# Performance work log

Hardware: AMD Instinct MI355X
Metric: run time of the kernel (lower is better)

Reference implementation:

```python
import jax, jax.numpy as jnp
import numpy as np

B, T, D, H = 2, 2048, 2048, 32
HD = D // H
# quantization scales (constructor-time attributes in the original repo)
A_PROJ = 3e-4   # q/k/v proj alpha (W8A8B8O8Linear)
A_QK = 2e-5     # qk_bmm alpha (BMM_S8T_S8N_F32T)
A_PV = 1e-2     # pv_bmm alpha (BMM_S8T_S8N_S8T)
A_OUT = 1e-4    # out_proj alpha (W8A8BFP32OFP32Linear)


def _i8(key, shape):
    return jax.random.randint(key, shape, -128, 128, dtype=jnp.int32).astype(jnp.int8)


def setup_inputs() -> dict:
    key = jax.random.key(0)
    ks = jax.random.split(key, 10)
    hidden_states = _i8(ks[0], (B, T, D))
    # causal mask, 0 on/below diagonal, large negative above
    causal = jnp.triu(jnp.full((T, T), -1e9, dtype=jnp.float32), k=1)
    attention_mask = jnp.broadcast_to(causal, (B, 1, T, T))
    return {
        "hidden_states": hidden_states,
        "attention_mask": attention_mask,
        "Wq": _i8(ks[1], (D, D)), "bq": _i8(ks[2], (D,)),
        "Wk": _i8(ks[3], (D, D)), "bk": _i8(ks[4], (D,)),
        "Wv": _i8(ks[5], (D, D)), "bv": _i8(ks[6], (D,)),
        "Wo": _i8(ks[7], (D, D)),
        "bo": jax.random.normal(ks[8], (D,), dtype=jnp.float32),
    }


def _w8a8b8o8(x_i8, W_i8, b_i8, alpha):
    # int8 GEMM -> int32 accum; epilogue: alpha*acc + bias, saturate to int8
    acc = jnp.einsum('btk,nk->btn', x_i8.astype(jnp.int32), W_i8.astype(jnp.int32))
    y = alpha * acc.astype(jnp.float32) + b_i8.astype(jnp.float32)
    return jnp.clip(jnp.round(y), -128, 127).astype(jnp.int8)


def reference(hidden_states, attention_mask, Wq, bq, Wk, bk, Wv, bv, Wo, bo):
    # q/k/v projections: int8 in, int8 out
    q = _w8a8b8o8(hidden_states, Wq, bq, A_PROJ)
    k = _w8a8b8o8(hidden_states, Wk, bk, A_PROJ)
    v = _w8a8b8o8(hidden_states, Wv, bv, A_PROJ)

    def shape(x):  # [B,T,D] -> [B,H,T,HD]
        return x.reshape(B, T, H, HD).transpose(0, 2, 1, 3)

    qh, kh, vh = shape(q), shape(k), shape(v)

    # qk_bmm (BMM_S8T_S8N_F32T): fp32 = alpha * int8 q @ k^T
    attn = A_QK * jnp.einsum('bhtd,bhsd->bhts',
                             qh.astype(jnp.int32), kh.astype(jnp.int32)).astype(jnp.float32)
    attn = attn + attention_mask  # [B,1,T,T] broadcasts over heads
    attn = jnp.maximum(attn, jnp.finfo(jnp.float32).min)
    probs = jax.nn.softmax(attn, axis=-1)

    # quantize probs: p.mul_(127).round_() -> int8
    p_i8 = jnp.clip(jnp.round(probs * 127.0), -128, 127).astype(jnp.int8)

    # pv_bmm (BMM_S8T_S8N_S8T): int8 out = sat(round(alpha * p @ v))
    pv = jnp.einsum('bhts,bhsd->bhtd', p_i8.astype(jnp.int32), vh.astype(jnp.int32))
    attn_out_i8 = jnp.clip(jnp.round(A_PV * pv.astype(jnp.float32)), -128, 127).astype(jnp.int8)

    # [B,H,T,HD] -> [B,T,D]
    attn_out = attn_out_i8.transpose(0, 2, 1, 3).reshape(B, T, D)

    # out_proj (W8A8BFP32OFP32Linear): fp32 = alpha*(x@W^T) + fp32 bias
    acc = jnp.einsum('btk,nk->btn', attn_out.astype(jnp.int32), Wo.astype(jnp.int32))
    out = A_OUT * acc.astype(jnp.float32) + bo
    return out
```

## Files before the change

kernel.cpp:

```cpp
#include <hip/hip_runtime.h>
#include <cstdint>

#define A_PROJ 3e-4f
#define A_QK   2e-5f
#define A_PV   1e-2f
#define A_OUT  1e-4f

#define NB 2
#define NT 2048
#define ND 2048
#define NH 32
#define NHD 64
#define NM (NB*NT)

typedef int v4i __attribute__((ext_vector_type(4)));

__device__ __forceinline__ int8_t sat8(float y) {
  float r = rintf(y);
  r = fminf(fmaxf(r, -128.f), 127.f);
  return (int8_t)(int)r;
}

__device__ __forceinline__ float exp2_fast(float x) {
  return __builtin_amdgcn_exp2f(x);
}

__device__ __forceinline__ void gl2lds16(const int8_t* g, int8_t* l) {
  __builtin_amdgcn_global_load_lds(
      (const __attribute__((address_space(1))) void*)g,
      (__attribute__((address_space(3))) void*)l, 16, 0, 0);
}

__device__ __forceinline__ uint32_t pack_lo4(float f0, float f1, float f2, float f3) {
  uint32_t u0 = __float_as_uint(f0), u1 = __float_as_uint(f1);
  uint32_t u2 = __float_as_uint(f2), u3 = __float_as_uint(f3);
  uint32_t lo = __builtin_amdgcn_perm(u1, u0, 0x04000400u);
  uint32_t hi = __builtin_amdgcn_perm(u3, u2, 0x04000400u);
  return __builtin_amdgcn_perm(hi, lo, 0x05040100u);
}

__device__ __forceinline__ void xcd_map(int lid, int& bx, int& by) {
  int xcd = lid & 7, j = lid >> 3;
  bx = (xcd & 3) * 8 + (j & 7);
  by = (xcd >> 2) * 8 + (j >> 3);
}

#define NWW (ND*ND/4)
__global__ void pack_all(const int* __restrict__ X,
                         const int* __restrict__ W0, const int* __restrict__ W1,
                         const int* __restrict__ W2, const int* __restrict__ W3,
                         int8_t* __restrict__ dX, int8_t* __restrict__ dW0,
                         int8_t* __restrict__ dW1, int8_t* __restrict__ dW2,
                         int8_t* __restrict__ dW3) {
  int i = blockIdx.x * blockDim.x + threadIdx.x;
  const int nx = NM*ND/4;
  const int* src; int8_t* dst; int off;
  if (i < nx) { src = X; dst = dX; off = i; }
  else {
    int j = i - nx;
    int r = j >> 20;
    off = j & (NWW - 1);
    src = (r == 0) ? W0 : (r == 1) ? W1 : (r == 2) ? W2 : W3;
    dst = (r == 0) ? dW0 : (r == 1) ? dW1 : (r == 2) ? dW2 : dW3;
  }
  int4 v = ((const int4*)src)[off];
  uint32_t p = (uint32_t)(v.x & 255) | ((uint32_t)(v.y & 255) << 8) |
               ((uint32_t)(v.z & 255) << 16) | ((uint32_t)(v.w & 255) << 24);
  ((uint32_t*)dst)[off] = p;
}

__global__ __launch_bounds__(256, 2) void gemm_qkv(
    const int8_t* __restrict__ X,
    const int8_t* __restrict__ Wq, const int8_t* __restrict__ Wk, const int8_t* __restrict__ Wv,
    const int* __restrict__ bq, const int* __restrict__ bk, const int* __restrict__ bv,
    int8_t* __restrict__ Qh, int8_t* __restrict__ Kh, int8_t* __restrict__ Vt)
{
  __shared__ __align__(16) int8_t S[2][4][128][64];
  int bx, by;
  xcd_map(blockIdx.x + 32 * blockIdx.y, bx, by);
  const int m0 = bx * 128, n0 = by * 128;
  const int tid = threadIdx.x, lane = tid & 63, wave = tid >> 6;
  const int wm = wave >> 1, wn = wave & 1;
  const int l15 = lane & 15, quad = lane >> 4;

  const int srow = lane >> 2;
  const int scol = (((lane & 3) ^ ((lane >> 3) & 3)) * 16);
  const int rqcol = (quad ^ ((l15 >> 1) & 3)) * 16;

  const int8_t* srcp[8];
  int8_t* dstp[8];
  #pragma unroll
  for (int j = 0; j < 8; ++j) {
    int slot = j * 4 + wave;
    int rblk = slot & 7;
    int sel  = slot >> 3;
    int row  = rblk * 16 + srow;
    const int8_t* base = (sel == 0) ? &X[(size_t)(m0 + row) * ND]
                                    : (sel == 1) ? &Wq[(size_t)(n0 + row) * ND]
                                    : (sel == 2) ? &Wk[(size_t)(n0 + row) * ND]
                                                 : &Wv[(size_t)(n0 + row) * ND];
    srcp[j] = base + scol;
    dstp[j] = &S[0][sel][rblk * 16][0];
  }

  v4i acc[3][4][4];
  const v4i vzero = {0, 0, 0, 0};
  #pragma unroll
  for (int z = 0; z < 3; ++z)
    #pragma unroll
    for (int i = 0; i < 4; ++i)
      #pragma unroll
      for (int j = 0; j < 4; ++j) acc[z][i][j] = vzero;

  #pragma unroll
  for (int j = 0; j < 8; ++j) gl2lds16(srcp[j], dstp[j]);
  __syncthreads();

  int cur = 0;
  for (int k0 = 64; k0 <= ND; k0 += 64) {
    if (k0 < ND) {
      const int boff = (cur ^ 1) * 32768;
      #pragma unroll
      for (int j = 0; j < 8; ++j) gl2lds16(srcp[j] + k0, dstp[j] + boff);
    }
    v4i a[4];
    #pragma unroll
    for (int mt = 0; mt < 4; ++mt)
      a[mt] = *(const v4i*)&S[cur][0][wm*64 + mt*16 + l15][rqcol];
    #pragma unroll
    for (int z = 0; z < 3; ++z)
      #pragma unroll
      for (int nt = 0; nt < 4; ++nt) {
        v4i b = *(const v4i*)&S[cur][1 + z][wn*64 + nt*16 + l15][rqcol];
        #pragma unroll
        for (int mt = 0; mt < 4; ++mt)
          acc[z][mt][nt] = __builtin_amdgcn_mfma_i32_16x16x64_i8(a[mt], b, acc[z][mt][nt], 0, 0, 0);
      }
    __syncthreads();
    cur ^= 1;
  }

  #pragma unroll
  for (int z = 0; z < 3; ++z) {
    const int* bias = (z == 0) ? bq : (z == 1) ? bk : bv;
    float bf[4];
    #pragma unroll
    for (int nt = 0; nt < 4; ++nt) bf[nt] = (float)bias[n0 + wn*64 + nt*16 + l15];
    if (z == 2) {
      #pragma unroll
      for (int mt = 0; mt < 4; ++mt)
        #pragma unroll
        for (int nt = 0; nt < 4; ++nt) {
          int tbase = (m0 + wm*64 + mt*16 + quad*4) & (NT - 1);
          int bb = (m0 + wm*64) >> 11;
          int n = n0 + wn*64 + nt*16 + l15;
          int hh = n >> 6, hd = n & (NHD - 1);
          uint32_t pk = 0;
          #pragma unroll
          for (int r = 0; r < 4; ++r) {
            uint32_t q = (uint32_t)(uint8_t)sat8(A_PROJ * (float)acc[z][mt][nt][r] + bf[nt]);
            pk |= q << (8 * r);
          }
          size_t bh = (size_t)bb * NH + hh;
          *(uint32_t*)&Vt[(bh * NHD + hd) * NT + tbase] = pk;
        }
    } else {
      int8_t* O = (z == 0) ? Qh : Kh;
      #pragma unroll
      for (int mt = 0; mt < 4; ++mt)
        #pragma unroll
        for (int nt = 0; nt < 4; ++nt)
          #pragma unroll
          for (int r = 0; r < 4; ++r) {
            int m = m0 + wm*64 + mt*16 + quad*4 + r;
            int n = n0 + wn*64 + nt*16 + l15;
            int8_t q = sat8(A_PROJ * (float)acc[z][mt][nt][r] + bf[nt]);
            int bb = m >> 11, t = m & (NT - 1);
            int hh = n >> 6, hd = n & (NHD - 1);
            size_t bh = (size_t)bb * NH + hh;
            O[(bh * NT + t) * NHD + hd] = q;
          }
    }
  }
}

__global__ __launch_bounds__(512, 8) void attn_fused(
    const int8_t* __restrict__ Qh, const int8_t* __restrict__ Kh, const int8_t* __restrict__ Vt,
    int8_t* __restrict__ AO)
{
  __shared__ __align__(16) int8_t Ksd[2][64][64];
  __shared__ __align__(16) int8_t Vsd[2][64][64];
  __shared__ __align__(16) uint32_t Ps32[8][16][20];

  const int bx = blockIdx.x;
  const int bh = blockIdx.y;
  const int tid = threadIdx.x, lane = tid & 63, wave = tid >> 6;
  const int l15 = lane & 15, quad = lane >> 4;
  const v4i vzero = {0, 0, 0, 0};
  const float MAGIC = 12582912.0f;
  const float C2 = 2.8853900817779268e-05f;

  const int jg = bh >> 4;
  const int x = (jg == 0) ? bx : (jg == 1) ? (15 - bx)
              : (jg == 2) ? ((bx + 8) & 15) : ((7 - bx) & 15);

  const int8_t* Qp = Qh + (size_t)bh * NT * NHD;
  const int8_t* Kp = Kh + (size_t)bh * NT * NHD;
  const int8_t* Vp = Vt + (size_t)bh * NHD * NT;
  const int bb = bh >> 5, hhead = bh & (NH - 1);

  const int t0 = x * 128;
  const int nsteps = 2 * x + 2;
  const int tw = t0 + wave * 16;
  const int tme = tw + l15;

  const int strow = lane >> 2;
  const int stcol = (((lane & 3) ^ ((lane >> 3) & 3)) * 16);
  const int fcol  = (quad ^ ((l15 >> 1) & 3)) * 16;

  v4i qf = *(const v4i*)&Qp[(size_t)(tw + l15) * NHD + quad * 16];

  float ls0 = 0.f, ls1 = 0.f, ls2 = 0.f, ls3 = 0.f;
  if (wave < 4)
    gl2lds16(&Kp[(size_t)(0 + wave*16 + strow) * NHD + stcol], &Ksd[0][wave*16][0]);
  __syncthreads();
  int cur = 0;
  for (int st = 0; st < nsteps; ++st) {
    if (st + 1 < nsteps && wave < 4)
      gl2lds16(&Kp[(size_t)((st+1)*64 + wave*16 + strow) * NHD + stcol],
               &Ksd[cur ^ 1][wave*16][0]);
    const int s0 = st * 64;
    if (s0 <= tw + 15) {
      v4i kf[4];
      #pragma unroll
      for (int mt = 0; mt < 4; ++mt) kf[mt] = *(const v4i*)&Ksd[cur][mt*16 + l15][fcol];
      if (s0 + 63 <= tw) {
        #pragma unroll
        for (int mt = 0; mt < 4; ++mt) {
          v4i sa = __builtin_amdgcn_mfma_i32_16x16x64_i8(kf[mt], qf, vzero, 0, 0, 0);
          ls0 += exp2_fast(C2 * (float)sa[0]);
          ls1 += exp2_fast(C2 * (float)sa[1]);
          ls2 += exp2_fast(C2 * (float)sa[2]);
          ls3 += exp2_fast(C2 * (float)sa[3]);
        }
      } else {
        #pragma unroll
        for (int mt = 0; mt < 4; ++mt) {
          v4i sa = __builtin_amdgcn_mfma_i32_16x16x64_i8(kf[mt], qf, vzero, 0, 0, 0);
          const int sb = s0 + mt*16 + quad*4;
          ls0 += (sb + 0 <= tme) ? exp2_fast(C2 * (float)sa[0]) : 0.f;
          ls1 += (sb + 1 <= tme) ? exp2_fast(C2 * (float)sa[1]) : 0.f;
          ls2 += (sb + 2 <= tme) ? exp2_fast(C2 * (float)sa[2]) : 0.f;
          ls3 += (sb + 3 <= tme) ? exp2_fast(C2 * (float)sa[3]) : 0.f;
        }
      }
    }
    __syncthreads();
    cur ^= 1;
  }
  float lsum = (ls0 + ls1) + (ls2 + ls3);
  lsum += __shfl_xor(lsum, 16, 64);
  lsum += __shfl_xor(lsum, 32, 64);
  const float linv = 127.0f / lsum;

  v4i accv[4];
  #pragma unroll
  for (int jj = 0; jj < 4; ++jj) accv[jj] = vzero;

  if (wave < 4)
    gl2lds16(&Kp[(size_t)(0 + wave*16 + strow) * NHD + stcol], &Ksd[0][wave*16][0]);
  else
    gl2lds16(&Vp[(size_t)((wave-4)*16 + strow) * NT + 0 + stcol], &Vsd[0][(wave-4)*16][0]);
  __syncthreads();
  cur = 0;
  for (int st = 0; st < nsteps; ++st) {
    if (st + 1 < nsteps) {
      if (wave < 4)
        gl2lds16(&Kp[(size_t)((st+1)*64 + wave*16 + strow) * NHD + stcol],
                 &Ksd[cur ^ 1][wave*16][0]);
      else
        gl2lds16(&Vp[(size_t)((wave-4)*16 + strow) * NT + (st+1)*64 + stcol],
                 &Vsd[cur ^ 1][(wave-4)*16][0]);
    }
    const int s0 = st * 64;
    if (s0 <= tw + 15) {
      v4i kf[4];
      #pragma unroll
      for (int mt = 0; mt < 4; ++mt) kf[mt] = *(const v4i*)&Ksd[cur][mt*16 + l15][fcol];
      if (s0 + 63 <= tw) {
        #pragma unroll
        for (int mt = 0; mt < 4; ++mt) {
          v4i sa = __builtin_amdgcn_mfma_i32_16x16x64_i8(kf[mt], qf, vzero, 0, 0, 0);
          float f0 = fmaf(exp2_fast(C2 * (float)sa[0]), linv, MAGIC);
          float f1 = fmaf(exp2_fast(C2 * (float)sa[1]), linv, MAGIC);
          float f2 = fmaf(exp2_fast(C2 * (float)sa[2]), linv, MAGIC);
          float f3 = fmaf(exp2_fast(C2 * (float)sa[3]), linv, MAGIC);
          Ps32[wave][l15][mt*4 + quad] = pack_lo4(f0, f1, f2, f3);
        }
      } else {
        #pragma unroll
        for (int mt = 0; mt < 4; ++mt) {
          v4i sa = __builtin_amdgcn_mfma_i32_16x16x64_i8(kf[mt], qf, vzero, 0, 0, 0);
          const int sb = s0 + mt*16 + quad*4;
          float e0 = (sb + 0 <= tme) ? exp2_fast(C2 * (float)sa[0]) : 0.f;
          float e1 = (sb + 1 <= tme) ? exp2_fast(C2 * (float)sa[1]) : 0.f;
          float e2 = (sb + 2 <= tme) ? exp2_fast(C2 * (float)sa[2]) : 0.f;
          float e3 = (sb + 3 <= tme) ? exp2_fast(C2 * (float)sa[3]) : 0.f;
          Ps32[wave][l15][mt*4 + quad] =
              pack_lo4(fmaf(e0, linv, MAGIC), fmaf(e1, linv, MAGIC),
                       fmaf(e2, linv, MAGIC), fmaf(e3, linv, MAGIC));
        }
      }
      v4i ap = *(const v4i*)&Ps32[wave][l15][quad*4];
      #pragma unroll
      for (int nt2 = 0; nt2 < 4; ++nt2) {
        v4i bvv = *(const v4i*)&Vsd[cur][nt2*16 + l15][fcol];
        accv[nt2] = __builtin_amdgcn_mfma_i32_16x16x64_i8(ap, bvv, accv[nt2], 0, 0, 0);
      }
    }
    __syncthreads();
    cur ^= 1;
  }

  #pragma unroll
  for (int nt2 = 0; nt2 < 4; ++nt2)
    #pragma unroll
    for (int r = 0; r < 4; ++r) {
      int t = tw + quad*4 + r;
      int d = nt2*16 + l15;
      AO[((size_t)bb * NT + t) * ND + hhead * NHD + d] = sat8(A_PV * (float)accv[nt2][r]);
    }
}

__global__ __launch_bounds__(256) void gemm_out(
    const int8_t* __restrict__ X, const int8_t* __restrict__ W,
    const float* __restrict__ bo, float* __restrict__ out)
{
  __shared__ __align__(16) int8_t As[2][128][64];
  __shared__ __align__(16) int8_t Bs[2][128][64];
  int bx, by;
  xcd_map(blockIdx.x + 32 * blockIdx.y, bx, by);
  const int m0 = bx * 128, n0 = by * 128;
  const int tid = threadIdx.x, lane = tid & 63, wave = tid >> 6;
  const int wm = wave >> 1, wn = wave & 1;
  const int l15 = lane & 15, quad = lane >> 4;
  const int srow = lane >> 2;
  const int scol = (((lane & 3) ^ ((lane >> 3) & 3)) * 16);
  const int rqcol = (quad ^ ((l15 >> 1) & 3)) * 16;

  const int8_t* srcp[4];
  int8_t* dstp[4];
  #pragma unroll
  for (int j = 0; j < 4; ++j) {
    int slot = j * 4 + wave;
    int rblk = slot & 7;
    int row = rblk * 16 + srow;
    if (slot < 8) { srcp[j] = &X[(size_t)(m0 + row) * ND + scol]; dstp[j] = &As[0][rblk*16][0]; }
    else          { srcp[j] = &W[(size_t)(n0 + row) * ND + scol]; dstp[j] = &Bs[0][rblk*16][0]; }
  }

  v4i acc[4][4];
  const v4i vzero = {0, 0, 0, 0};
  #pragma unroll
  for (int i = 0; i < 4; ++i)
    #pragma unroll
    for (int j = 0; j < 4; ++j) acc[i][j] = vzero;

  #pragma unroll
  for (int j = 0; j < 4; ++j) gl2lds16(srcp[j], dstp[j]);
  __syncthreads();

  int cur = 0;
  for (int k0 = 64; k0 <= ND; k0 += 64) {
    if (k0 < ND) {
      const int boff = (cur ^ 1) * 8192;
      #pragma unroll
      for (int j = 0; j < 4; ++j) gl2lds16(srcp[j] + k0, dstp[j] + boff);
    }
    v4i a[4], b[4];
    #pragma unroll
    for (int mt = 0; mt < 4; ++mt) a[mt] = *(const v4i*)&As[cur][wm*64 + mt*16 + l15][rqcol];
    #pragma unroll
    for (int nt = 0; nt < 4; ++nt) b[nt] = *(const v4i*)&Bs[cur][wn*64 + nt*16 + l15][rqcol];
    #pragma unroll
    for (int mt = 0; mt < 4; ++mt)
      #pragma unroll
      for (int nt = 0; nt < 4; ++nt)
        acc[mt][nt] = __builtin_amdgcn_mfma_i32_16x16x64_i8(a[mt], b[nt], acc[mt][nt], 0, 0, 0);
    __syncthreads();
    cur ^= 1;
  }

  float bf[4];
  #pragma unroll
  for (int nt = 0; nt < 4; ++nt) bf[nt] = bo[n0 + wn*64 + nt*16 + l15];

  #pragma unroll
  for (int mt = 0; mt < 4; ++mt)
    #pragma unroll
    for (int nt = 0; nt < 4; ++nt)
      #pragma unroll
      for (int r = 0; r < 4; ++r) {
        int m = m0 + wm*64 + mt*16 + quad*4 + r;
        int n = n0 + wn*64 + nt*16 + l15;
        out[(size_t)m * ND + n] = A_OUT * (float)acc[mt][nt][r] + bf[nt];
      }
}

extern "C" void kernel_launch(void* const* d_in, const int* in_sizes, int n_in,
                              void* d_out, int out_size, void* d_ws, size_t ws_size,
                              hipStream_t stream)
{
  const int*   hs  = (const int*)d_in[0];
  const int*   Wq  = (const int*)d_in[2];
  const int*   bq  = (const int*)d_in[3];
  const int*   Wk  = (const int*)d_in[4];
  const int*   bkb = (const int*)d_in[5];
  const int*   Wv  = (const int*)d_in[6];
  const int*   bvb = (const int*)d_in[7];
  const int*   Wo  = (const int*)d_in[8];
  const float* bo  = (const float*)d_in[9];
  float* out = (float*)d_out;

  char* ws = (char*)d_ws;
  const size_t SZ_X = (size_t)NM * ND;
  const size_t SZ_W = (size_t)ND * ND;
  const size_t SZ_H = (size_t)NB * NH * NT * NHD;
  int8_t* Xp  = (int8_t*)ws;
  int8_t* Wqp = (int8_t*)(ws + SZ_X);
  int8_t* Wkp = Wqp + SZ_W;
  int8_t* Wvp = Wkp + SZ_W;
  int8_t* Wop = Wvp + SZ_W;
  int8_t* Qh  = Wop + SZ_W;
  int8_t* Kh  = Qh + SZ_H;
  int8_t* Vt  = Kh + SZ_H;
  int8_t* AO  = Xp;

  const int ntot = (int)(SZ_X/4 + 4 * (SZ_W/4));
  pack_all<<<(ntot + 255) / 256, 256, 0, stream>>>(hs, Wq, Wk, Wv, Wo,
                                                   Xp, Wqp, Wkp, Wvp, Wop);

  gemm_qkv<<<dim3(32, 16), 256, 0, stream>>>(Xp, Wqp, Wkp, Wvp, bq, bkb, bvb, Qh, Kh, Vt);
  attn_fused<<<dim3(16, NB*NH), 512, 0, stream>>>(Qh, Kh, Vt, AO);
  gemm_out<<<dim3(NM/128, ND/128), 256, 0, stream>>>(AO, Wop, bo, out);
}
```

Baseline: 304.4 us.

## Restructure attention blocks into paired 64-row query tiles for causal balance

Each attention block now has 256 threads (4 waves) and handles two 64-row query tiles, bx and 31-bx. Pairing them gives every block the same total causal work, replacing the previous per-head-group swizzle over 128-row tiles. All waves now load both K and V, and the per-wave skip check is no longer needed because tiles match the 64-wide key step. The trade-offs are a smaller block with fewer waves to hide latency and two serial passes per block.

Measured after the change: 308.8 us. Within noise of the previous version (+1.4%).

```diff
diff --git a/kernel.cpp b/kernel.cpp
--- a/kernel.cpp
+++ b/kernel.cpp
@@ -184,13 +184,13 @@
   }
 }
 
-__global__ __launch_bounds__(512, 8) void attn_fused(
+__global__ __launch_bounds__(256, 4) void attn_fused(
     const int8_t* __restrict__ Qh, const int8_t* __restrict__ Kh, const int8_t* __restrict__ Vt,
     int8_t* __restrict__ AO)
 {
   __shared__ __align__(16) int8_t Ksd[2][64][64];
   __shared__ __align__(16) int8_t Vsd[2][64][64];
-  __shared__ __align__(16) uint32_t Ps32[8][16][20];
+  __shared__ __align__(16) uint32_t Ps32[4][16][20];
 
   const int bx = blockIdx.x;
   const int bh = blockIdx.y;
@@ -200,50 +200,36 @@
   const float MAGIC = 12582912.0f;
   const float C2 = 2.8853900817779268e-05f;
 
-  const int jg = bh >> 4;
-  const int x = (jg == 0) ? bx : (jg == 1) ? (15 - bx)
-              : (jg == 2) ? ((bx + 8) & 15) : ((7 - bx) & 15);
-
   const int8_t* Qp = Qh + (size_t)bh * NT * NHD;
   const int8_t* Kp = Kh + (size_t)bh * NT * NHD;
   const int8_t* Vp = Vt + (size_t)bh * NHD * NT;
   const int bb = bh >> 5, hhead = bh & (NH - 1);
 
-  const int t0 = x * 128;
-  const int nsteps = 2 * x + 2;
-  const int tw = t0 + wave * 16;
-  const int tme = tw + l15;
-
   const int strow = lane >> 2;
   const int stcol = (((lane & 3) ^ ((lane >> 3) & 3)) * 16);
   const int fcol  = (quad ^ ((l15 >> 1) & 3)) * 16;
 
-  v4i qf = *(const v4i*)&Qp[(size_t)(tw + l15) * NHD + quad * 16];
-
-  float ls0 = 0.f, ls1 = 0.f, ls2 = 0.f, ls3 = 0.f;
-  if (wave < 4)
-    gl2lds16(&Kp[(size_t)(0 + wave*16 + strow) * NHD + stcol], &Ksd[0][wave*16][0]);
-  __syncthreads();
-  int cur = 0;
-  for (int st = 0; st < nsteps; ++st) {
-    if (st + 1 < nsteps && wave < 4)
-      gl2lds16(&Kp[(size_t)((st+1)*64 + wave*16 + strow) * NHD + stcol],
-               &Ksd[cur ^ 1][wave*16][0]);
-    const int s0 = st * 64;
-    if (s0 <= tw + 15) {
+  for (int half = 0; half < 2; ++half) {
+    const int x = half ? (31 - bx) : bx;
+    const int t0 = x * 64;
+    const int tw = t0 + wave * 16;
+    const int tme = tw + l15;
+
+    v4i qf = *(const v4i*)&Qp[(size_t)(tw + l15) * NHD + quad * 16];
+
+    float ls0 = 0.f, ls1 = 0.f, ls2 = 0.f, ls3 = 0.f;
+    gl2lds16(&Kp[(size_t)(wave*16 + strow) * NHD + stcol], &Ksd[0][wave*16][0]);
+    __syncthreads();
+    int cur = 0;
+    for (int st = 0; st <= x; ++st) {
+      if (st < x)
+        gl2lds16(&Kp[(size_t)((st+1)*64 + wave*16 + strow) * NHD + stcol],
+                 &Ksd[cur ^ 1][wave*16][0]);
+      const int s0 = st * 64;
       v4i kf[4];
       #pragma unroll
       for (int mt = 0; mt < 4; ++mt) kf[mt] = *(const v4i*)&Ksd[cur][mt*16 + l15][fcol];
-      if (s0 + 63 <= tw) {
-        #pragma unroll
-        for (int mt = 0; mt < 4; ++mt) {
-          v4i sa = __builtin_amdgcn_mfma_i32_16x16x64_i8(kf[mt], qf, vzero, 0, 0, 0);
-          ls0 += exp2_fast(C2 * (float)sa[0]);
-          ls1 += exp2_fast(C2 * (float)sa[1]);
-          ls2 += exp2_fast(C2 * (float)sa[2]);
-          ls3 += exp2_fast(C2 * (float)sa[3]);
-        }
-      } else {
+      if (st == x) {
         #pragma unroll
         for (int mt = 0; mt < 4; ++mt) {
           v4i sa = __builtin_amdgcn_mfma_i32_16x16x64_i8(kf[mt], qf, vzero, 0, 0, 0);
@@ -253,51 +239,44 @@
           ls2 += (sb + 2 <= tme) ? exp2_fast(C2 * (float)sa[2]) : 0.f;
           ls3 += (sb + 3 <= tme) ? exp2_fast(C2 * (float)sa[3]) : 0.f;
         }
-      }
+      } else {
+        #pragma unroll
+        for (int mt = 0; mt < 4; ++mt) {
+          v4i sa = __builtin_amdgcn_mfma_i32_16x16x64_i8(kf[mt], qf, vzero, 0, 0, 0);
+          ls0 += exp2_fast(C2 * (float)sa[0]);
+          ls1 += exp2_fast(C2 * (float)sa[1]);
+          ls2 += exp2_fast(C2 * (float)sa[2]);
+          ls3 += exp2_fast(C2 * (float)sa[3]);
+        }
+      }
+      __syncthreads();
+      cur ^= 1;
     }
+    float lsum = (ls0 + ls1) + (ls2 + ls3);
+    lsum += __shfl_xor(lsum, 16, 64);
+    lsum += __shfl_xor(lsum, 32, 64);
+    const float linv = 127.0f / lsum;
+
+    v4i accv[4];
+    #pragma unroll
+    for (int jj = 0; jj < 4; ++jj) accv[jj] = vzero;
+
+    gl2lds16(&Kp[(size_t)(wave*16 + strow) * NHD + stcol], &Ksd[0][wave*16][0]);
+    gl2lds16(&Vp[(size_t)(wave*16 + strow) * NT + stcol], &Vsd[0][wave*16][0]);
     __syncthreads();
-    cur ^= 1;
-  }
-  float lsum = (ls0 + ls1) + (ls2 + ls3);
-  lsum += __shfl_xor(lsum, 16, 64);
-  lsum += __shfl_xor(lsum, 32, 64);
-  const float linv = 127.0f / lsum;
-
-  v4i accv[4];
-  #pragma unroll
-  for (int jj = 0; jj < 4; ++jj) accv[jj] = vzero;
-
-  if (wave < 4)
-    gl2lds16(&Kp[(size_t)(0 + wave*16 + strow) * NHD + stcol], &Ksd[0][wave*16][0]);
-  else
-    gl2lds16(&Vp[(size_t)((wave-4)*16 + strow) * NT + 0 + stcol], &Vsd[0][(wave-4)*16][0]);
-  __syncthreads();
-  cur = 0;
-  for (int st = 0; st < nsteps; ++st) {
-    if (st + 1 < nsteps) {
-      if (wave < 4)
+    cur = 0;
+    for (int st = 0; st <= x; ++st) {
+      if (st < x) {
         gl2lds16(&Kp[(size_t)((st+1)*64 + wave*16 + strow) * NHD + stcol],
                  &Ksd[cur ^ 1][wave*16][0]);
-      else
-        gl2lds16(&Vp[(size_t)((wave-4)*16 + strow) * NT + (st+1)*64 + stcol],
-                 &Vsd[cur ^ 1][(wave-4)*16][0]);
-    }
-    const int s0 = st * 64;
-    if (s0 <= tw + 15) {
+        gl2lds16(&Vp[(size_t)(wave*16 + strow) * NT + (st+1)*64 + stcol],
+                 &Vsd[cur ^ 1][wave*16][0]);
+      }
+      const int s0 = st * 64;
       v4i kf[4];
       #pragma unroll
       for (int mt = 0; mt < 4; ++mt) kf[mt] = *(const v4i*)&Ksd[cur][mt*16 + l15][fcol];
-      if (s0 + 63 <= tw) {
-        #pragma unroll
-        for (int mt = 0; mt < 4; ++mt) {
-          v4i sa = __builtin_amdgcn_mfma_i32_16x16x64_i8(kf[mt], qf, vzero, 0, 0, 0);
-          float f0 = fmaf(exp2_fast(C2 * (float)sa[0]), linv, MAGIC);
-          float f1 = fmaf(exp2_fast(C2 * (float)sa[1]), linv, MAGIC);
-          float f2 = fmaf(exp2_fast(C2 * (float)sa[2]), linv, MAGIC);
-          float f3 = fmaf(exp2_fast(C2 * (float)sa[3]), linv, MAGIC);
-          Ps32[wave][l15][mt*4 + quad] = pack_lo4(f0, f1, f2, f3);
-        }
-      } else {
+      if (st == x) {
         #pragma unroll
         for (int mt = 0; mt < 4; ++mt) {
           v4i sa = __builtin_amdgcn_mfma_i32_16x16x64_i8(kf[mt], qf, vzero, 0, 0, 0);
@@ -310,6 +289,16 @@
               pack_lo4(fmaf(e0, linv, MAGIC), fmaf(e1, linv, MAGIC),
                        fmaf(e2, linv, MAGIC), fmaf(e3, linv, MAGIC));
         }
+      } else {
+        #pragma unroll
+        for (int mt = 0; mt < 4; ++mt) {
+          v4i sa = __builtin_amdgcn_mfma_i32_16x16x64_i8(kf[mt], qf, vzero, 0, 0, 0);
+          float f0 = fmaf(exp2_fast(C2 * (float)sa[0]), linv, MAGIC);
+          float f1 = fmaf(exp2_fast(C2 * (float)sa[1]), linv, MAGIC);
+          float f2 = fmaf(exp2_fast(C2 * (float)sa[2]), linv, MAGIC);
+          float f3 = fmaf(exp2_fast(C2 * (float)sa[3]), linv, MAGIC);
+          Ps32[wave][l15][mt*4 + quad] = pack_lo4(f0, f1, f2, f3);
+        }
       }
       v4i ap = *(const v4i*)&Ps32[wave][l15][quad*4];
       #pragma unroll
@@ -317,19 +306,19 @@
         v4i bvv = *(const v4i*)&Vsd[cur][nt2*16 + l15][fcol];
         accv[nt2] = __builtin_amdgcn_mfma_i32_16x16x64_i8(ap, bvv, accv[nt2], 0, 0, 0);
       }
+      __syncthreads();
+      cur ^= 1;
     }
-    __syncthreads();
-    cur ^= 1;
-  }
-
-  #pragma unroll
-  for (int nt2 = 0; nt2 < 4; ++nt2)
-    #pragma unroll
-    for (int r = 0; r < 4; ++r) {
-      int t = tw + quad*4 + r;
-      int d = nt2*16 + l15;
-      AO[((size_t)bb * NT + t) * ND + hhead * NHD + d] = sat8(A_PV * (float)accv[nt2][r]);
-    }
+
+    #pragma unroll
+    for (int nt2 = 0; nt2 < 4; ++nt2)
+      #pragma unroll
+      for (int r = 0; r < 4; ++r) {
+        int t = tw + quad*4 + r;
+        int d = nt2*16 + l15;
+        AO[((size_t)bb * NT + t) * ND + hhead * NHD + d] = sat8(A_PV * (float)accv[nt2][r]);
+      }
+  }
 }
 
 __global__ __launch_bounds__(256) void gemm_out(
@@ -441,6 +430,6 @@
                                                    Xp, Wqp, Wkp, Wvp, Wop);
 
   gemm_qkv<<<dim3(32, 16), 256, 0, stream>>>(Xp, Wqp, Wkp, Wvp, bq, bkb, bvb, Qh, Kh, Vt);
-  attn_fused<<<dim3(16, NB*NH), 512, 0, stream>>>(Qh, Kh, Vt, AO);
+  attn_fused<<<dim3(16, NB*NH), 256, 0, stream>>>(Qh, Kh, Vt, AO);
   gemm_out<<<dim3(NM/128, ND/128), 256, 0, stream>>>(AO, Wop, bo, out);
 }
```
